# Kernel optimization log

Measured on AMD Instinct MI355X. Metric: run time of the kernel, lower is better.

The kernel has to match this reference:

```python
import jax, jax.numpy as jnp
import numpy as np

_FP8_MAX = 448.0  # finfo(float8_e4m3fn).max


def _quantize_fp8(w):
    """Per-tensor FP8 quantization: returns fp8-snapped weight (as f32) and scale."""
    scale = jnp.maximum(jnp.max(jnp.abs(w)).astype(jnp.float32) / _FP8_MAX, 1e-12)
    w_q = (w / scale).astype(jnp.float8_e4m3fn).astype(jnp.float32)
    return w_q, scale


def setup_inputs() -> dict:
    key = jax.random.key(0)
    k_x, k_g, k_u, k_d = jax.random.split(key, 4)
    B, S, H, I = 4, 2048, 4096, 11008
    x = jax.random.normal(k_x, (B, S, H), dtype=jnp.float32)
    gate = jax.random.normal(k_g, (I, H), dtype=jnp.float32) * 0.05
    up = jax.random.normal(k_u, (I, H), dtype=jnp.float32) * 0.05
    down = jax.random.normal(k_d, (H, I), dtype=jnp.float32) * 0.05
    gate_w, gate_w_scale = _quantize_fp8(gate)
    up_w, up_w_scale = _quantize_fp8(up)
    down_w, down_w_scale = _quantize_fp8(down)
    one = jnp.float32(1.0)
    return {
        "x": x,
        "gate_w": gate_w, "up_w": up_w, "down_w": down_w,
        "gate_w_scale": gate_w_scale, "up_w_scale": up_w_scale, "down_w_scale": down_w_scale,
        "gate_in_scale": one, "up_in_scale": one, "down_in_scale": one,
    }


def _fake_quant_fp8_linear(x, w_q, in_scale, w_scale):
    # Fake-quantize activations to FP8 (per-tensor scale), dequantize weight, GEMM.
    x_q = jnp.clip(x / in_scale, -_FP8_MAX, _FP8_MAX)
    x_dq = x_q.astype(jnp.float8_e4m3fn).astype(jnp.float32) * in_scale
    w_dq = w_q * w_scale  # w_q values are already on the FP8 grid
    return jnp.einsum('bsh,ih->bsi', x_dq, w_dq)


def reference(x, gate_w, up_w, down_w, gate_w_scale, up_w_scale, down_w_scale,
              gate_in_scale, up_in_scale, down_in_scale):
    gate_out = _fake_quant_fp8_linear(x, gate_w, gate_in_scale, gate_w_scale)
    up_out = _fake_quant_fp8_linear(x, up_w, up_in_scale, up_w_scale)
    hidden = jax.nn.silu(gate_out) * up_out  # SwiGLU
    return _fake_quant_fp8_linear(hidden, down_w, down_in_scale, down_w_scale)
```

## Files before the change

### kernel.cpp

```cpp
#include <hip/hip_runtime.h>
#include <stdint.h>


typedef float f32x4 __attribute__((ext_vector_type(4)));
typedef int   i32x4 __attribute__((ext_vector_type(4)));
typedef int   i32x8 __attribute__((ext_vector_type(8)));
typedef unsigned int u32;

#define AS1 __attribute__((address_space(1)))
#define AS3 __attribute__((address_space(3)))

#define TM 128
#define TN 128
#define BKB 128

#define SCALE1 0x7F7F7F7F

__device__ __forceinline__ void gld_lds16(const uint8_t* g, uint8_t* l) {
  __builtin_amdgcn_global_load_lds((const AS1 u32*)g, (AS3 u32*)l, 16, 0, 0);
}

__device__ __forceinline__ uint8_t f32_to_fp8(float v) {
  v = fminf(fmaxf(v, -448.f), 448.f);
  int r = __builtin_amdgcn_cvt_pk_fp8_f32(v, v, 0, false);
  return (uint8_t)(r & 0xff);
}

__device__ __forceinline__ i32x8 read_frag32(const uint8_t* s, int row, int ko, int swz) {
  const uint8_t* p = s + row * BKB;
  i32x4 lo = *(const i32x4*)(p + ((ko) ^ swz));
  i32x4 hi = *(const i32x4*)(p + ((ko + 16) ^ swz));
  return __builtin_shufflevector(lo, hi, 0, 1, 2, 3, 4, 5, 6, 7);
}

__global__ __launch_bounds__(256) void quant_fp8_k(const float* __restrict__ in,
                                                   uint8_t* __restrict__ out,
                                                   const float* __restrict__ scale_ptr,
                                                   long n8) {
  long i = (long)blockIdx.x * 256 + threadIdx.x;
  if (i >= n8) return;
  float inv = scale_ptr ? (1.0f / scale_ptr[0]) : 1.0f;
  const float4* p = (const float4*)(in + i * 8);
  float4 a = p[0], b = p[1];
  float v0 = fminf(fmaxf(a.x * inv, -448.f), 448.f);
  float v1 = fminf(fmaxf(a.y * inv, -448.f), 448.f);
  float v2 = fminf(fmaxf(a.z * inv, -448.f), 448.f);
  float v3 = fminf(fmaxf(a.w * inv, -448.f), 448.f);
  float v4 = fminf(fmaxf(b.x * inv, -448.f), 448.f);
  float v5 = fminf(fmaxf(b.y * inv, -448.f), 448.f);
  float v6 = fminf(fmaxf(b.z * inv, -448.f), 448.f);
  float v7 = fminf(fmaxf(b.w * inv, -448.f), 448.f);
  int lo = __builtin_amdgcn_cvt_pk_fp8_f32(v0, v1, 0, false);
  lo = __builtin_amdgcn_cvt_pk_fp8_f32(v2, v3, lo, true);
  int hi = __builtin_amdgcn_cvt_pk_fp8_f32(v4, v5, 0, false);
  hi = __builtin_amdgcn_cvt_pk_fp8_f32(v6, v7, hi, true);
  ((int2*)out)[i] = make_int2(lo, hi);
}

__global__ __launch_bounds__(256, 2) void gemm1_swiglu(
    const uint8_t* __restrict__ Xq,
    const uint8_t* __restrict__ Gq,
    const uint8_t* __restrict__ Uq,
    uint8_t* __restrict__ Hq,
    const float* __restrict__ gws, const float* __restrict__ uws,
    const float* __restrict__ gis, const float* __restrict__ uis,
    const float* __restrict__ dis,
    int M, int H, int I) {
  __shared__ uint8_t sX[TM * BKB];
  __shared__ uint8_t sG[2][TN * BKB];
  __shared__ uint8_t sU[2][TN * BKB];

  const int tid = threadIdx.x;
  const int wave = tid >> 6, lane = tid & 63;
  const int wr = wave >> 1, wc = wave & 1;
  const int lrow = lane & 15;
  const int lkg = lane >> 4;
  const int swz = (lrow & 7) << 4;
  const int ko = lkg * 32;

  const int GX = 43, GY = 16;
  const int per = GX * GY;
  const int g = blockIdx.x / per, w = blockIdx.x % per;
  const int ggx = g & 1, ggy = g >> 1;
  const int xb = ggx * GX + w / GY;
  const int yb = ggy * GY + (w % GY);
  const int bM = yb * TM, bN = xb * TN;

  f32x4 accG[4][4] = {};
  f32x4 accU[4][4] = {};

  const uint8_t* gx = Xq + (size_t)bM * H;
  const uint8_t* gg = Gq + (size_t)bN * H;
  const uint8_t* gu = Uq + (size_t)bN * H;

  auto stageX = [&](int k0) {
#pragma unroll
    for (int it = 0; it < 4; ++it) {
      int c = it * 256 + tid;
      int r = c >> 3;
      int col = ((c & 7) ^ (r & 7)) * 16;
      gld_lds16(gx + (size_t)r * H + k0 + col, sX + (it * 4 + wave) * 1024);
    }
  };
  auto stageGU = [&](int buf, int k0) {
#pragma unroll
    for (int it = 0; it < 4; ++it) {
      int c = it * 256 + tid;
      int r = c >> 3;
      int col = ((c & 7) ^ (r & 7)) * 16;
      size_t go = (size_t)r * H + k0 + col;
      int lo = (it * 4 + wave) * 1024;
      gld_lds16(gg + go, &sG[buf][lo]);
      gld_lds16(gu + go, &sU[buf][lo]);
    }
  };

  const int NK = H / BKB;
  stageGU(0, 0);

  for (int t = 0; t < NK; ++t) {
    const int cur = t & 1, nxt = cur ^ 1;
    stageX(t * BKB);
    if (t + 1 < NK) {
      stageGU(nxt, (t + 1) * BKB);
      asm volatile("s_waitcnt vmcnt(8)" ::: "memory");
    } else {
      asm volatile("s_waitcnt vmcnt(0)" ::: "memory");
    }
    __builtin_amdgcn_s_barrier();

    i32x8 af[4];
#pragma unroll
    for (int i = 0; i < 4; ++i)
      af[i] = read_frag32(sX, wr * 64 + i * 16 + lrow, ko, swz);
#pragma unroll
    for (int j = 0; j < 4; ++j) {
      i32x8 gf = read_frag32(&sG[cur][0], wc * 64 + j * 16 + lrow, ko, swz);
      i32x8 uf = read_frag32(&sU[cur][0], wc * 64 + j * 16 + lrow, ko, swz);
#pragma unroll
      for (int i = 0; i < 4; ++i) {
        accG[i][j] = __builtin_amdgcn_mfma_scale_f32_16x16x128_f8f6f4(
            af[i], gf, accG[i][j], 0, 0, 0, SCALE1, 0, SCALE1);
        accU[i][j] = __builtin_amdgcn_mfma_scale_f32_16x16x128_f8f6f4(
            af[i], uf, accU[i][j], 0, 0, 0, SCALE1, 0, SCALE1);
      }
    }
    asm volatile("s_waitcnt lgkmcnt(0)" ::: "memory");
    __builtin_amdgcn_s_barrier();
  }

  const float sg = gws[0] * gis[0];
  const float su = uws[0] * uis[0];
  const float invd = 1.0f / dis[0];

  uint8_t* sH = sX;

#pragma unroll
  for (int i = 0; i < 4; ++i)
#pragma unroll
    for (int j = 0; j < 4; ++j)
#pragma unroll
      for (int t = 0; t < 4; ++t) {
        float g2 = accG[i][j][t] * sg;
        float u = accU[i][j][t] * su;
        float h = (g2 / (1.0f + expf(-g2))) * u * invd;
        int row = wr * 64 + i * 16 + lkg * 4 + t;
        int col = wc * 64 + j * 16 + lrow;
        sH[row * TN + col] = f32_to_fp8(h);
      }
  __syncthreads();
#pragma unroll
  for (int it = 0; it < 4; ++it) {
    int o = (it * 256 + tid) * 16;
    int row = o >> 7, col = o & 127;
    *(int4*)(Hq + (size_t)(bM + row) * I + bN + col) = *(const int4*)(sH + o);
  }
}

__global__ __launch_bounds__(256, 2) void gemm2_down(
    const uint8_t* __restrict__ Hq,
    const uint8_t* __restrict__ Dq,
    float* __restrict__ Out,
    const float* __restrict__ dws, const float* __restrict__ dis,
    int M, int I, int Hd) {
  __shared__ uint8_t sA[TM * BKB];
  __shared__ uint8_t sB[2][2 * TN * BKB];

  const int tid = threadIdx.x;
  const int wave = tid >> 6, lane = tid & 63;
  const int wr = wave >> 1, wc = wave & 1;
  const int lrow = lane & 15;
  const int lkg = lane >> 4;
  const int swz = (lrow & 7) << 4;
  const int ko = lkg * 32;

  const int g = blockIdx.x >> 8, w = blockIdx.x & 255;
  const int xb = w >> 4;
  const int yb = (g << 4) + (w & 15);
  const int bM = yb * TM, bN = xb * 256;

  f32x4 acc[4][8] = {};

  const uint8_t* ga = Hq + (size_t)bM * I;
  const uint8_t* gb = Dq + (size_t)bN * I;

  auto stageA = [&](int k0) {
#pragma unroll
    for (int it = 0; it < 4; ++it) {
      int c = it * 256 + tid;
      int r = c >> 3;
      int col = ((c & 7) ^ (r & 7)) * 16;
      gld_lds16(ga + (size_t)r * I + k0 + col, sA + (it * 4 + wave) * 1024);
    }
  };
  auto stageB = [&](int buf, int k0) {
#pragma unroll
    for (int it = 0; it < 8; ++it) {
      int c = it * 256 + tid;
      int r = c >> 3;
      int col = ((c & 7) ^ (r & 7)) * 16;
      gld_lds16(gb + (size_t)r * I + k0 + col, &sB[buf][(it * 4 + wave) * 1024]);
    }
  };

  const int NK = I / BKB;
  stageB(0, 0);

  for (int t = 0; t < NK; ++t) {
    const int cur = t & 1, nxt = cur ^ 1;
    stageA(t * BKB);
    if (t + 1 < NK) {
      stageB(nxt, (t + 1) * BKB);
      asm volatile("s_waitcnt vmcnt(8)" ::: "memory");
    } else {
      asm volatile("s_waitcnt vmcnt(0)" ::: "memory");
    }
    __builtin_amdgcn_s_barrier();

    i32x8 af[4];
#pragma unroll
    for (int i = 0; i < 4; ++i)
      af[i] = read_frag32(sA, wr * 64 + i * 16 + lrow, ko, swz);
#pragma unroll
    for (int j = 0; j < 8; ++j) {
      i32x8 bf = read_frag32(&sB[cur][0], wc * 128 + j * 16 + lrow, ko, swz);
#pragma unroll
      for (int i = 0; i < 4; ++i)
        acc[i][j] = __builtin_amdgcn_mfma_scale_f32_16x16x128_f8f6f4(
            af[i], bf, acc[i][j], 0, 0, 0, SCALE1, 0, SCALE1);
    }
    asm volatile("s_waitcnt lgkmcnt(0)" ::: "memory");
    __builtin_amdgcn_s_barrier();
  }

  const float ds = dws[0] * dis[0];
#pragma unroll
  for (int i = 0; i < 4; ++i)
#pragma unroll
    for (int j = 0; j < 8; ++j) {
      int row = bM + wr * 64 + i * 16 + lkg * 4;
      int col = bN + wc * 128 + j * 16 + lrow;
#pragma unroll
      for (int t = 0; t < 4; ++t)
        Out[(size_t)(row + t) * Hd + col] = acc[i][j][t] * ds;
    }
}

extern "C" void kernel_launch(void* const* d_in, const int* in_sizes, int n_in,
                              void* d_out, int out_size, void* d_ws, size_t ws_size,
                              hipStream_t stream) {
  const float* x   = (const float*)d_in[0];
  const float* gw  = (const float*)d_in[1];
  const float* uw  = (const float*)d_in[2];
  const float* dw  = (const float*)d_in[3];
  const float* gws = (const float*)d_in[4];
  const float* uws = (const float*)d_in[5];
  const float* dws = (const float*)d_in[6];
  const float* gis = (const float*)d_in[7];
  const float* uis = (const float*)d_in[8];
  const float* dis = (const float*)d_in[9];

  const int Hd = 4096;
  const int M  = in_sizes[0] / Hd;
  const int I  = in_sizes[1] / Hd;

  const size_t szX = (size_t)M * Hd;
  const size_t szW = (size_t)I * Hd;
  const size_t szH = (size_t)M * I;

  uint8_t* xq = (uint8_t*)d_ws;
  uint8_t* gq = xq + szX;
  uint8_t* uq = gq + szW;
  uint8_t* hq = uq + szW;
  uint8_t* dq = gq;

  if (ws_size < szX + 2 * szW + szH) return;

  float* out = (float*)d_out;

  {
    long n8 = (long)(szX / 8);
    quant_fp8_k<<<dim3((n8 + 255) / 256), dim3(256), 0, stream>>>(x, xq, gis, n8);
  }
  {
    long n8 = (long)(szW / 8);
    quant_fp8_k<<<dim3((n8 + 255) / 256), dim3(256), 0, stream>>>(gw, gq, nullptr, n8);
    quant_fp8_k<<<dim3((n8 + 255) / 256), dim3(256), 0, stream>>>(uw, uq, nullptr, n8);
  }

  gemm1_swiglu<<<dim3((I / TN) * (M / TM)), dim3(256), 0, stream>>>(
      xq, gq, uq, hq, gws, uws, gis, uis, dis, M, Hd, I);

  {
    long n8 = (long)(szW / 8);
    quant_fp8_k<<<dim3((n8 + 255) / 256), dim3(256), 0, stream>>>(dw, dq, nullptr, n8);
  }
  gemm2_down<<<dim3((Hd / 256) * (M / TM)), dim3(256), 0, stream>>>(
      hq, dq, out, dws, dis, M, I, Hd);
}
```

Before: 1.174 ms.

## Prefetch A/X tiles through registers to overlap loads with MFMA

The X (and hidden) tile was previously loaded straight into LDS in the same iteration it was consumed, so each step waited on its own global load. Both GEMM kernels now load the next iteration's A tile into registers, then write it to LDS after the compute barrier, which gives A a full iteration of latency hiding. The cost is extra VGPRs, possibly lower occupancy, added LDS store instructions, and a waitcnt count that must stay correct. Since the compiler may also insert its own vmcnt waits for the register loads, the manual vmcnt(12) may not control the overlap as intended.

New measurement: 2.109 ms. +79.6%, slower.

```diff
diff --git a/kernel.cpp b/kernel.cpp
--- a/kernel.cpp
+++ b/kernel.cpp
@@ -93,14 +93,23 @@
   const uint8_t* gg = Gq + (size_t)bN * H;
   const uint8_t* gu = Uq + (size_t)bN * H;
 
-  auto stageX = [&](int k0) {
+  int4 xr0, xr1, xr2, xr3;
+  auto loadXreg = [&](int k0) {
 #pragma unroll
     for (int it = 0; it < 4; ++it) {
       int c = it * 256 + tid;
       int r = c >> 3;
       int col = ((c & 7) ^ (r & 7)) * 16;
-      gld_lds16(gx + (size_t)r * H + k0 + col, sX + (it * 4 + wave) * 1024);
-    }
+      const int4 v = *(const int4*)(gx + (size_t)r * H + k0 + col);
+      if (it == 0) xr0 = v; else if (it == 1) xr1 = v;
+      else if (it == 2) xr2 = v; else xr3 = v;
+    }
+  };
+  auto writeXlds = [&]() {
+    *(int4*)(sX + (0 * 4 + wave) * 1024 + lane * 16) = xr0;
+    *(int4*)(sX + (1 * 4 + wave) * 1024 + lane * 16) = xr1;
+    *(int4*)(sX + (2 * 4 + wave) * 1024 + lane * 16) = xr2;
+    *(int4*)(sX + (3 * 4 + wave) * 1024 + lane * 16) = xr3;
   };
   auto stageGU = [&](int buf, int k0) {
 #pragma unroll
@@ -116,17 +125,22 @@
   };
 
   const int NK = H / BKB;
+
+  loadXreg(0);
   stageGU(0, 0);
+  writeXlds();
 
   for (int t = 0; t < NK; ++t) {
     const int cur = t & 1, nxt = cur ^ 1;
-    stageX(t * BKB);
-    if (t + 1 < NK) {
+    const bool pre = (t + 1 < NK);
+    if (pre) {
+      loadXreg((t + 1) * BKB);
       stageGU(nxt, (t + 1) * BKB);
-      asm volatile("s_waitcnt vmcnt(8)" ::: "memory");
+      asm volatile("s_waitcnt vmcnt(12)" ::: "memory");
     } else {
       asm volatile("s_waitcnt vmcnt(0)" ::: "memory");
     }
+    asm volatile("s_waitcnt lgkmcnt(0)" ::: "memory");
     __builtin_amdgcn_s_barrier();
 
     i32x8 af[4];
@@ -147,6 +161,7 @@
     }
     asm volatile("s_waitcnt lgkmcnt(0)" ::: "memory");
     __builtin_amdgcn_s_barrier();
+    if (pre) writeXlds();
   }
 
   const float sg = gws[0] * gis[0];
@@ -204,14 +219,23 @@
   const uint8_t* ga = Hq + (size_t)bM * I;
   const uint8_t* gb = Dq + (size_t)bN * I;
 
-  auto stageA = [&](int k0) {
+  int4 ar0, ar1, ar2, ar3;
+  auto loadAreg = [&](int k0) {
 #pragma unroll
     for (int it = 0; it < 4; ++it) {
       int c = it * 256 + tid;
       int r = c >> 3;
       int col = ((c & 7) ^ (r & 7)) * 16;
-      gld_lds16(ga + (size_t)r * I + k0 + col, sA + (it * 4 + wave) * 1024);
-    }
+      const int4 v = *(const int4*)(ga + (size_t)r * I + k0 + col);
+      if (it == 0) ar0 = v; else if (it == 1) ar1 = v;
+      else if (it == 2) ar2 = v; else ar3 = v;
+    }
+  };
+  auto writeAlds = [&]() {
+    *(int4*)(sA + (0 * 4 + wave) * 1024 + lane * 16) = ar0;
+    *(int4*)(sA + (1 * 4 + wave) * 1024 + lane * 16) = ar1;
+    *(int4*)(sA + (2 * 4 + wave) * 1024 + lane * 16) = ar2;
+    *(int4*)(sA + (3 * 4 + wave) * 1024 + lane * 16) = ar3;
   };
   auto stageB = [&](int buf, int k0) {
 #pragma unroll
@@ -224,17 +248,22 @@
   };
 
   const int NK = I / BKB;
+
+  loadAreg(0);
   stageB(0, 0);
+  writeAlds();
 
   for (int t = 0; t < NK; ++t) {
     const int cur = t & 1, nxt = cur ^ 1;
-    stageA(t * BKB);
-    if (t + 1 < NK) {
+    const bool pre = (t + 1 < NK);
+    if (pre) {
+      loadAreg((t + 1) * BKB);
       stageB(nxt, (t + 1) * BKB);
-      asm volatile("s_waitcnt vmcnt(8)" ::: "memory");
+      asm volatile("s_waitcnt vmcnt(12)" ::: "memory");
     } else {
       asm volatile("s_waitcnt vmcnt(0)" ::: "memory");
     }
+    asm volatile("s_waitcnt lgkmcnt(0)" ::: "memory");
     __builtin_amdgcn_s_barrier();
 
     i32x8 af[4];
@@ -251,6 +280,7 @@
     }
     asm volatile("s_waitcnt lgkmcnt(0)" ::: "memory");
     __builtin_amdgcn_s_barrier();
+    if (pre) writeAlds();
   }
 
   const float ds = dws[0] * dis[0];
```
